# Optimization experiments

Hardware: AMD Instinct MI355X
Metric: run time of the kernel (lower is better)

The kernel has to match this reference:

```python
import jax, jax.numpy as jnp
import numpy as np
import math

EMBED_DIM = 256
NUM_HEADS = 8
HEAD_DIM = EMBED_DIM // NUM_HEADS
SEQ = 512
BSZ = 2


def setup_inputs() -> dict:
    key = jax.random.key(0)
    ks = jax.random.split(key, 9)
    def xavier(k, shape):
        fan_in, fan_out = shape[1], shape[0]
        bound = math.sqrt(6.0 / (fan_in + fan_out))
        return jax.random.uniform(k, shape, jnp.float32, -bound, bound)
    return {
        "query": jax.random.normal(ks[0], (SEQ, BSZ, EMBED_DIM), jnp.float32),
        "key": jax.random.normal(ks[1], (SEQ, BSZ, EMBED_DIM), jnp.float32),
        "value": jax.random.normal(ks[2], (SEQ, BSZ, EMBED_DIM), jnp.float32),
        "rel_pos_embedding": jax.random.normal(ks[3], (BSZ, SEQ, SEQ, EMBED_DIM), jnp.float32),
        "attn_mask": jax.random.normal(ks[4], (SEQ, SEQ), jnp.float32),
        "in_proj_weight": xavier(ks[5], (3 * EMBED_DIM, EMBED_DIM)),
        "in_proj_bias": jnp.zeros((3 * EMBED_DIM,), jnp.float32),
        "out_proj_weight": xavier(ks[6], (EMBED_DIM, EMBED_DIM)),
        "out_proj_bias": jnp.zeros((EMBED_DIM,), jnp.float32),
    }


def reference(query, key, value, rel_pos_embedding, attn_mask,
              in_proj_weight, in_proj_bias, out_proj_weight, out_proj_bias):
    L, B, E = query.shape
    H, D = NUM_HEADS, HEAD_DIM
    # NOTE: original module projects ONLY the query and chunks into q,k,v
    qkv = query @ in_proj_weight.T + in_proj_bias          # (L,B,3E)
    q, k, v = jnp.split(qkv, 3, axis=-1)                    # each (L,B,E)
    # (L,B,E) -> (B*H, L, D)
    def to_heads(t):
        return jnp.swapaxes(t.reshape(L, B * H, D), 0, 1)
    q, k, v = to_heads(q), to_heads(k), to_heads(v)
    scores = jnp.einsum('nld,nmd->nlm', q, k) / math.sqrt(D)  # (B*H,L,L)
    # relative position bias: einsum over UNSCALED q
    q4 = q.reshape(B, H, L, D)
    rel = rel_pos_embedding.reshape(B, L, L, H, D)
    rel_bias = jnp.einsum('bhld,blmhd->bhlm', q4, rel)        # (B,H,L,L)
    scores = scores.reshape(B, H, L, L) + rel_bias
    # additive 2D attn_mask broadcast over batch and heads
    scores = scores + attn_mask[None, None, :, :]
    scores = scores.reshape(B * H, L, L)
    attn = jax.nn.softmax(scores, axis=-1)                    # (B*H,L,L)
    out = jnp.einsum('nlm,nmd->nld', attn, v)                 # (B*H,L,D)
    out = jnp.swapaxes(out, 0, 1).reshape(L, B, E)            # (L,B,E)
    out = out @ out_proj_weight.T + out_proj_bias
    return out, attn
```

## Files before the change

### kernel.cpp

```cpp
#include <hip/hip_runtime.h>
#include <math.h>

#define L_SEQ 512
#define BSZ 2
#define NH 8
#define HD 32
#define E 256
#define SCALE 0.17677669529663687f
#define SROW 520

typedef float f32x4 __attribute__((ext_vector_type(4)));

template <int CTRL>
__device__ __forceinline__ float dpp_add(float x) {
    return x + __int_as_float(
        __builtin_amdgcn_update_dpp(0, __float_as_int(x), CTRL, 0xF, 0xF, true));
}
__device__ __forceinline__ float octet_allsum(float x) {
    x = dpp_add<0xB1>(x);
    x = dpp_add<0x4E>(x);
    x = dpp_add<0x141>(x);
    return x;
}


__global__ void inproj_kernel(const float* __restrict__ query,
                              const float* __restrict__ W,
                              const float* __restrict__ bias,
                              float* __restrict__ q2,
                              float* __restrict__ kh,
                              float* __restrict__ vh) {
    int r0 = blockIdx.x * 4;
    int y  = blockIdx.y;
    int t = threadIdx.x;
    __shared__ float xs[4][E];
#pragma unroll
    for (int r = 0; r < 4; ++r) xs[r][t] = query[(size_t)(r0 + r) * E + t];
    __syncthreads();

    int c = t & 7, cg = t >> 3;
#pragma unroll
    for (int pp = 0; pp < 4; ++pp) {
        int pass = y * 4 + pp;
        int col = pass * 32 + cg;
        float a[3][4];
#pragma unroll
        for (int p = 0; p < 3; ++p)
#pragma unroll
            for (int r = 0; r < 4; ++r) a[p][r] = 0.f;

#pragma unroll
        for (int kk = 0; kk < 8; ++kk) {
            float4 x0 = ((const float4*)xs[0])[c + kk * 8];
            float4 x1 = ((const float4*)xs[1])[c + kk * 8];
            float4 x2 = ((const float4*)xs[2])[c + kk * 8];
            float4 x3 = ((const float4*)xs[3])[c + kk * 8];
#pragma unroll
            for (int p = 0; p < 3; ++p) {
                float4 w = ((const float4*)(W + (size_t)(p * E + col) * E))[c + kk * 8];
                a[p][0] += w.x * x0.x + w.y * x0.y + w.z * x0.z + w.w * x0.w;
                a[p][1] += w.x * x1.x + w.y * x1.y + w.z * x1.z + w.w * x1.w;
                a[p][2] += w.x * x2.x + w.y * x2.y + w.z * x2.z + w.w * x2.w;
                a[p][3] += w.x * x3.x + w.y * x3.y + w.z * x3.z + w.w * x3.w;
            }
        }
#pragma unroll
        for (int p = 0; p < 3; ++p)
#pragma unroll
            for (int r = 0; r < 4; ++r) a[p][r] = octet_allsum(a[p][r]);

        if (c == 0) {
#pragma unroll
            for (int p = 0; p < 3; ++p) {
                float bb = bias[p * E + col];
#pragma unroll
                for (int r = 0; r < 4; ++r) {
                    int row = r0 + r, l = row >> 1, b = row & 1;
                    float val = a[p][r] + bb;
                    if (p == 0) {
                        q2[((size_t)b * L_SEQ + l) * E + col] = val;
                    } else {
                        int h = col >> 5, d = col & 31;
                        float* dst = (p == 1) ? kh : vh;
                        dst[((size_t)(b * NH + h) * L_SEQ + l) * HD + d] = val;
                    }
                }
            }
        }
    }
}

__global__ void qk_kernel(const float* __restrict__ q2,
                          const float* __restrict__ kh,
                          const float* __restrict__ mask,
                          float* __restrict__ scores) {
    int n = blockIdx.x;
    int b = n >> 3, h = n & 7;
    int l0 = blockIdx.y * 32;
    int t = threadIdx.x, lane = t & 63, w = t >> 6;

    __shared__ float qs[32][32];
    {
        int row = t >> 3, quad = t & 7;
        float4 qv = *(const float4*)(q2 + ((size_t)b * L_SEQ + l0 + row) * E + h * HD + quad * 4);
        ((float4*)qs[row])[quad] = qv;
    }
    __syncthreads();

    f32x4 ka[8], kb[8];
    const float* kbase = kh + (size_t)n * L_SEQ * HD;
    {
        const f32x4* pa = (const f32x4*)(kbase + (size_t)(w * 128 + lane) * HD);
        const f32x4* pb = (const f32x4*)(kbase + (size_t)(w * 128 + 64 + lane) * HD);
#pragma unroll
        for (int i = 0; i < 8; ++i) { ka[i] = pa[i]; kb[i] = pb[i]; }
    }

    for (int li = 0; li < 32; ++li) {
        int l = l0 + li;
        float da = 0.f, db = 0.f;
#pragma unroll
        for (int i = 0; i < 8; ++i) {
            float4 qv = ((const float4*)qs[li])[i];
            da += ka[i].x * qv.x + ka[i].y * qv.y + ka[i].z * qv.z + ka[i].w * qv.w;
            db += kb[i].x * qv.x + kb[i].y * qv.y + kb[i].z * qv.z + kb[i].w * qv.w;
        }
        size_t off = ((size_t)n * L_SEQ + l) * L_SEQ;
        const float* mrow = mask + (size_t)l * L_SEQ;
        scores[off + w * 128 + lane]      = da * SCALE + mrow[w * 128 + lane];
        scores[off + w * 128 + 64 + lane] = db * SCALE + mrow[w * 128 + 64 + lane];
    }
}

__global__ void attn_kernel(const float* __restrict__ q2,
                            const float* __restrict__ vh,
                            const float* __restrict__ rpe,
                            const float* __restrict__ scores,
                            float* __restrict__ attn_out,
                            float* __restrict__ oh2) {
    int bid = blockIdx.x;
    int b = bid >> 9, l = bid & (L_SEQ - 1);
    int t = threadIdx.x;
    int lane = t & 63, wid = t >> 6;

    __shared__ float qs[E];
    __shared__ float s_lds[NH * SROW];

    if (t < E) qs[t] = q2[((size_t)b * L_SEQ + l) * E + t];
    __syncthreads();

    f32x4 qc = ((const f32x4*)qs)[lane];
    int csel = lane & 7, h1 = lane >> 3;
    const float* rbase = rpe + ((size_t)(b * L_SEQ + l)) * L_SEQ * E;

    for (int ii = 0; ii < 8; ++ii) {
        float keep = 0.f;
#pragma unroll
        for (int i8 = 0; i8 < 8; ++i8) {
            int m = wid * 64 + ii * 8 + i8;
            f32x4 rv = __builtin_nontemporal_load(((const f32x4*)(rbase + (size_t)m * E)) + lane);
            float part = rv.x * qc.x + rv.y * qc.y + rv.z * qc.z + rv.w * qc.w;
            part = octet_allsum(part);
            keep = (i8 == csel) ? part : keep;
        }
        s_lds[h1 * SROW + wid * 64 + ii * 8 + csel] = keep;
    }
    __syncthreads();

    int h = wid;
    const float* srow = scores + ((size_t)(b * NH + h) * L_SEQ + l) * L_SEQ;
    float sv[8];
    float mx = -1e30f;
#pragma unroll
    for (int i = 0; i < 8; ++i) {
        int m = i * 64 + lane;
        sv[i] = s_lds[h * SROW + m] + srow[m];
        mx = fmaxf(mx, sv[i]);
    }
#pragma unroll
    for (int off = 32; off > 0; off >>= 1) mx = fmaxf(mx, __shfl_xor(mx, off));
    float sum = 0.f;
#pragma unroll
    for (int i = 0; i < 8; ++i) { sv[i] = __expf(sv[i] - mx); sum += sv[i]; }
#pragma unroll
    for (int off = 32; off > 0; off >>= 1) sum += __shfl_xor(sum, off);
    float inv = 1.0f / sum;

    float* arow = attn_out + ((size_t)(b * NH + h) * L_SEQ + l) * L_SEQ;
#pragma unroll
    for (int i = 0; i < 8; ++i) {
        int m = i * 64 + lane;
        float pn = sv[i] * inv;
        arow[m] = pn;
        s_lds[h * SROW + m] = pn;
    }

    int dq = lane & 7, mg = lane >> 3;
    const f32x4* vbase = (const f32x4*)(vh + (size_t)(b * NH + h) * L_SEQ * HD);
    float4 acc = {0.f, 0.f, 0.f, 0.f};
#pragma unroll 4
    for (int i = 0; i < 64; ++i) {
        int m = i * 8 + mg;
        f32x4 v4 = vbase[(size_t)m * 8 + dq];
        float p = s_lds[h * SROW + m];
        acc.x += p * v4.x; acc.y += p * v4.y; acc.z += p * v4.z; acc.w += p * v4.w;
    }
#pragma unroll
    for (int off = 8; off <= 32; off <<= 1) {
        acc.x += __shfl_xor(acc.x, off);
        acc.y += __shfl_xor(acc.y, off);
        acc.z += __shfl_xor(acc.z, off);
        acc.w += __shfl_xor(acc.w, off);
    }
    if (mg == 0) {
        ((float4*)(oh2 + ((size_t)b * L_SEQ + l) * E))[h * 8 + dq] = acc;
    }
}

__global__ void outproj_kernel(const float* __restrict__ oh2,
                               const float* __restrict__ W,
                               const float* __restrict__ bias,
                               float* __restrict__ out) {
    int r0 = blockIdx.x * 4;
    int y  = blockIdx.y;
    int t = threadIdx.x;
    __shared__ float xs[4][E];
#pragma unroll
    for (int r = 0; r < 4; ++r) {
        int row = r0 + r, l = row >> 1, b = row & 1;
        xs[r][t] = oh2[((size_t)b * L_SEQ + l) * E + t];
    }
    __syncthreads();

    int c = t & 7, cg = t >> 3;
#pragma unroll
    for (int pp = 0; pp < 4; ++pp) {
        int pass = y * 4 + pp;
        int col = pass * 32 + cg;
        const float4* wp = (const float4*)(W + (size_t)col * E);
        float a0 = 0.f, a1 = 0.f, a2 = 0.f, a3 = 0.f;
#pragma unroll
        for (int kk = 0; kk < 8; ++kk) {
            float4 w  = wp[c + kk * 8];
            float4 x0 = ((const float4*)xs[0])[c + kk * 8];
            float4 x1 = ((const float4*)xs[1])[c + kk * 8];
            float4 x2 = ((const float4*)xs[2])[c + kk * 8];
            float4 x3 = ((const float4*)xs[3])[c + kk * 8];
            a0 += w.x * x0.x + w.y * x0.y + w.z * x0.z + w.w * x0.w;
            a1 += w.x * x1.x + w.y * x1.y + w.z * x1.z + w.w * x1.w;
            a2 += w.x * x2.x + w.y * x2.y + w.z * x2.z + w.w * x2.w;
            a3 += w.x * x3.x + w.y * x3.y + w.z * x3.z + w.w * x3.w;
        }
        a0 = octet_allsum(a0); a1 = octet_allsum(a1);
        a2 = octet_allsum(a2); a3 = octet_allsum(a3);
        if (c == 0) {
            float bb = bias[col];
            float res[4] = {a0, a1, a2, a3};
#pragma unroll
            for (int r = 0; r < 4; ++r) {
                out[(size_t)(r0 + r) * E + col] = res[r] + bb;
            }
        }
    }
}

extern "C" void kernel_launch(void* const* d_in, const int* in_sizes, int n_in,
                              void* d_out, int out_size, void* d_ws, size_t ws_size,
                              hipStream_t stream) {
    const float* query = (const float*)d_in[0];
    const float* rpe   = (const float*)d_in[3];
    const float* mask  = (const float*)d_in[4];
    const float* Win   = (const float*)d_in[5];
    const float* bin   = (const float*)d_in[6];
    const float* Wout  = (const float*)d_in[7];
    const float* bout  = (const float*)d_in[8];

    float* out  = (float*)d_out;
    float* attn = (float*)d_out + (size_t)L_SEQ * BSZ * E;

    float* q2     = (float*)d_ws;
    float* kh     = q2  + (size_t)BSZ * L_SEQ * E;
    float* vh     = kh  + (size_t)BSZ * NH * L_SEQ * HD;
    float* oh2    = vh  + (size_t)BSZ * NH * L_SEQ * HD;
    float* scores = oh2 + (size_t)BSZ * L_SEQ * E;

    inproj_kernel<<<dim3((L_SEQ * BSZ) / 4, 2), E, 0, stream>>>(query, Win, bin, q2, kh, vh);
    qk_kernel<<<dim3(BSZ * NH, L_SEQ / 32), 256, 0, stream>>>(q2, kh, mask, scores);
    attn_kernel<<<BSZ * L_SEQ, 512, 0, stream>>>(q2, vh, rpe, scores, attn, oh2);
    outproj_kernel<<<dim3((L_SEQ * BSZ) / 4, 2), E, 0, stream>>>(oh2, Wout, bout, out);
}
```

Measured before the change: 188.5 us.

## Split PV out of attention kernel, widen projection grids, simplify rel-pos reduction

Moves the attention-times-V product out of the fused attention kernel into a separate pv_kernel. The new kernel stages V in LDS with a swizzle and re-reads the attn rows that were just written. The in/out projection and QK kernels get more blocks with less work each, and DPP octet sums are replaced by shfl_xor. The rel-pos loop now uses plain loads instead of nontemporal loads and writes from one lane per octet. The rpe stream is still the dominant cost, and the extra launch plus the attn re-read add traffic.

```diff
diff --git a/kernel.cpp b/kernel.cpp
--- a/kernel.cpp
+++ b/kernel.cpp
@@ -11,18 +11,6 @@
 
 typedef float f32x4 __attribute__((ext_vector_type(4)));
 
-template <int CTRL>
-__device__ __forceinline__ float dpp_add(float x) {
-    return x + __int_as_float(
-        __builtin_amdgcn_update_dpp(0, __float_as_int(x), CTRL, 0xF, 0xF, true));
-}
-__device__ __forceinline__ float octet_allsum(float x) {
-    x = dpp_add<0xB1>(x);
-    x = dpp_add<0x4E>(x);
-    x = dpp_add<0x141>(x);
-    return x;
-}
-
 
 __global__ void inproj_kernel(const float* __restrict__ query,
                               const float* __restrict__ W,
@@ -30,214 +18,19 @@
                               float* __restrict__ q2,
                               float* __restrict__ kh,
                               float* __restrict__ vh) {
-    int r0 = blockIdx.x * 4;
-    int y  = blockIdx.y;
+    int rg = blockIdx.x;
+    int cg3 = blockIdx.y;
     int t = threadIdx.x;
     __shared__ float xs[4][E];
 #pragma unroll
-    for (int r = 0; r < 4; ++r) xs[r][t] = query[(size_t)(r0 + r) * E + t];
+    for (int r = 0; r < 4; ++r) xs[r][t] = query[(size_t)(rg * 4 + r) * E + t];
     __syncthreads();
 
     int c = t & 7, cg = t >> 3;
 #pragma unroll
-    for (int pp = 0; pp < 4; ++pp) {
-        int pass = y * 4 + pp;
-        int col = pass * 32 + cg;
-        float a[3][4];
-#pragma unroll
-        for (int p = 0; p < 3; ++p)
-#pragma unroll
-            for (int r = 0; r < 4; ++r) a[p][r] = 0.f;
-
-#pragma unroll
-        for (int kk = 0; kk < 8; ++kk) {
-            float4 x0 = ((const float4*)xs[0])[c + kk * 8];
-            float4 x1 = ((const float4*)xs[1])[c + kk * 8];
-            float4 x2 = ((const float4*)xs[2])[c + kk * 8];
-            float4 x3 = ((const float4*)xs[3])[c + kk * 8];
-#pragma unroll
-            for (int p = 0; p < 3; ++p) {
-                float4 w = ((const float4*)(W + (size_t)(p * E + col) * E))[c + kk * 8];
-                a[p][0] += w.x * x0.x + w.y * x0.y + w.z * x0.z + w.w * x0.w;
-                a[p][1] += w.x * x1.x + w.y * x1.y + w.z * x1.z + w.w * x1.w;
-                a[p][2] += w.x * x2.x + w.y * x2.y + w.z * x2.z + w.w * x2.w;
-                a[p][3] += w.x * x3.x + w.y * x3.y + w.z * x3.z + w.w * x3.w;
-            }
-        }
-#pragma unroll
-        for (int p = 0; p < 3; ++p)
-#pragma unroll
-            for (int r = 0; r < 4; ++r) a[p][r] = octet_allsum(a[p][r]);
-
-        if (c == 0) {
-#pragma unroll
-            for (int p = 0; p < 3; ++p) {
-                float bb = bias[p * E + col];
-#pragma unroll
-                for (int r = 0; r < 4; ++r) {
-                    int row = r0 + r, l = row >> 1, b = row & 1;
-                    float val = a[p][r] + bb;
-                    if (p == 0) {
-                        q2[((size_t)b * L_SEQ + l) * E + col] = val;
-                    } else {
-                        int h = col >> 5, d = col & 31;
-                        float* dst = (p == 1) ? kh : vh;
-                        dst[((size_t)(b * NH + h) * L_SEQ + l) * HD + d] = val;
-                    }
-                }
-            }
-        }
-    }
-}
-
-__global__ void qk_kernel(const float* __restrict__ q2,
-                          const float* __restrict__ kh,
-                          const float* __restrict__ mask,
-                          float* __restrict__ scores) {
-    int n = blockIdx.x;
-    int b = n >> 3, h = n & 7;
-    int l0 = blockIdx.y * 32;
-    int t = threadIdx.x, lane = t & 63, w = t >> 6;
-
-    __shared__ float qs[32][32];
-    {
-        int row = t >> 3, quad = t & 7;
-        float4 qv = *(const float4*)(q2 + ((size_t)b * L_SEQ + l0 + row) * E + h * HD + quad * 4);
-        ((float4*)qs[row])[quad] = qv;
-    }
-    __syncthreads();
-
-    f32x4 ka[8], kb[8];
-    const float* kbase = kh + (size_t)n * L_SEQ * HD;
-    {
-        const f32x4* pa = (const f32x4*)(kbase + (size_t)(w * 128 + lane) * HD);
-        const f32x4* pb = (const f32x4*)(kbase + (size_t)(w * 128 + 64 + lane) * HD);
-#pragma unroll
-        for (int i = 0; i < 8; ++i) { ka[i] = pa[i]; kb[i] = pb[i]; }
-    }
-
-    for (int li = 0; li < 32; ++li) {
-        int l = l0 + li;
-        float da = 0.f, db = 0.f;
-#pragma unroll
-        for (int i = 0; i < 8; ++i) {
-            float4 qv = ((const float4*)qs[li])[i];
-            da += ka[i].x * qv.x + ka[i].y * qv.y + ka[i].z * qv.z + ka[i].w * qv.w;
-            db += kb[i].x * qv.x + kb[i].y * qv.y + kb[i].z * qv.z + kb[i].w * qv.w;
-        }
-        size_t off = ((size_t)n * L_SEQ + l) * L_SEQ;
-        const float* mrow = mask + (size_t)l * L_SEQ;
-        scores[off + w * 128 + lane]      = da * SCALE + mrow[w * 128 + lane];
-        scores[off + w * 128 + 64 + lane] = db * SCALE + mrow[w * 128 + 64 + lane];
-    }
-}
-
-__global__ void attn_kernel(const float* __restrict__ q2,
-                            const float* __restrict__ vh,
-                            const float* __restrict__ rpe,
-                            const float* __restrict__ scores,
-                            float* __restrict__ attn_out,
-                            float* __restrict__ oh2) {
-    int bid = blockIdx.x;
-    int b = bid >> 9, l = bid & (L_SEQ - 1);
-    int t = threadIdx.x;
-    int lane = t & 63, wid = t >> 6;
-
-    __shared__ float qs[E];
-    __shared__ float s_lds[NH * SROW];
-
-    if (t < E) qs[t] = q2[((size_t)b * L_SEQ + l) * E + t];
-    __syncthreads();
-
-    f32x4 qc = ((const f32x4*)qs)[lane];
-    int csel = lane & 7, h1 = lane >> 3;
-    const float* rbase = rpe + ((size_t)(b * L_SEQ + l)) * L_SEQ * E;
-
-    for (int ii = 0; ii < 8; ++ii) {
-        float keep = 0.f;
-#pragma unroll
-        for (int i8 = 0; i8 < 8; ++i8) {
-            int m = wid * 64 + ii * 8 + i8;
-            f32x4 rv = __builtin_nontemporal_load(((const f32x4*)(rbase + (size_t)m * E)) + lane);
-            float part = rv.x * qc.x + rv.y * qc.y + rv.z * qc.z + rv.w * qc.w;
-            part = octet_allsum(part);
-            keep = (i8 == csel) ? part : keep;
-        }
-        s_lds[h1 * SROW + wid * 64 + ii * 8 + csel] = keep;
-    }
-    __syncthreads();
-
-    int h = wid;
-    const float* srow = scores + ((size_t)(b * NH + h) * L_SEQ + l) * L_SEQ;
-    float sv[8];
-    float mx = -1e30f;
-#pragma unroll
-    for (int i = 0; i < 8; ++i) {
-        int m = i * 64 + lane;
-        sv[i] = s_lds[h * SROW + m] + srow[m];
-        mx = fmaxf(mx, sv[i]);
-    }
-#pragma unroll
-    for (int off = 32; off > 0; off >>= 1) mx = fmaxf(mx, __shfl_xor(mx, off));
-    float sum = 0.f;
-#pragma unroll
-    for (int i = 0; i < 8; ++i) { sv[i] = __expf(sv[i] - mx); sum += sv[i]; }
-#pragma unroll
-    for (int off = 32; off > 0; off >>= 1) sum += __shfl_xor(sum, off);
-    float inv = 1.0f / sum;
-
-    float* arow = attn_out + ((size_t)(b * NH + h) * L_SEQ + l) * L_SEQ;
-#pragma unroll
-    for (int i = 0; i < 8; ++i) {
-        int m = i * 64 + lane;
-        float pn = sv[i] * inv;
-        arow[m] = pn;
-        s_lds[h * SROW + m] = pn;
-    }
-
-    int dq = lane & 7, mg = lane >> 3;
-    const f32x4* vbase = (const f32x4*)(vh + (size_t)(b * NH + h) * L_SEQ * HD);
-    float4 acc = {0.f, 0.f, 0.f, 0.f};
-#pragma unroll 4
-    for (int i = 0; i < 64; ++i) {
-        int m = i * 8 + mg;
-        f32x4 v4 = vbase[(size_t)m * 8 + dq];
-        float p = s_lds[h * SROW + m];
-        acc.x += p * v4.x; acc.y += p * v4.y; acc.z += p * v4.z; acc.w += p * v4.w;
-    }
-#pragma unroll
-    for (int off = 8; off <= 32; off <<= 1) {
-        acc.x += __shfl_xor(acc.x, off);
-        acc.y += __shfl_xor(acc.y, off);
-        acc.z += __shfl_xor(acc.z, off);
-        acc.w += __shfl_xor(acc.w, off);
-    }
-    if (mg == 0) {
-        ((float4*)(oh2 + ((size_t)b * L_SEQ + l) * E))[h * 8 + dq] = acc;
-    }
-}
-
-__global__ void outproj_kernel(const float* __restrict__ oh2,
-                               const float* __restrict__ W,
-                               const float* __restrict__ bias,
-                               float* __restrict__ out) {
-    int r0 = blockIdx.x * 4;
-    int y  = blockIdx.y;
-    int t = threadIdx.x;
-    __shared__ float xs[4][E];
-#pragma unroll
-    for (int r = 0; r < 4; ++r) {
-        int row = r0 + r, l = row >> 1, b = row & 1;
-        xs[r][t] = oh2[((size_t)b * L_SEQ + l) * E + t];
-    }
-    __syncthreads();
-
-    int c = t & 7, cg = t >> 3;
-#pragma unroll
-    for (int pp = 0; pp < 4; ++pp) {
-        int pass = y * 4 + pp;
-        int col = pass * 32 + cg;
-        const float4* wp = (const float4*)(W + (size_t)col * E);
+    for (int pp = 0; pp < 2; ++pp) {
+        int col768 = cg3 * 64 + pp * 32 + cg;
+        const float4* wp = (const float4*)(W + (size_t)col768 * E);
         float a0 = 0.f, a1 = 0.f, a2 = 0.f, a3 = 0.f;
 #pragma unroll
         for (int kk = 0; kk < 8; ++kk) {
@@ -251,14 +44,234 @@
             a2 += w.x * x2.x + w.y * x2.y + w.z * x2.z + w.w * x2.w;
             a3 += w.x * x3.x + w.y * x3.y + w.z * x3.z + w.w * x3.w;
         }
-        a0 = octet_allsum(a0); a1 = octet_allsum(a1);
-        a2 = octet_allsum(a2); a3 = octet_allsum(a3);
+#pragma unroll
+        for (int off = 1; off <= 4; off <<= 1) {
+            a0 += __shfl_xor(a0, off);
+            a1 += __shfl_xor(a1, off);
+            a2 += __shfl_xor(a2, off);
+            a3 += __shfl_xor(a3, off);
+        }
+        if (c == 0) {
+            int p = col768 >> 8, col = col768 & 255;
+            float bb = bias[col768];
+            float res[4] = {a0, a1, a2, a3};
+#pragma unroll
+            for (int r = 0; r < 4; ++r) {
+                int row = rg * 4 + r, l = row >> 1, b = row & 1;
+                float val = res[r] + bb;
+                if (p == 0) {
+                    q2[((size_t)b * L_SEQ + l) * E + col] = val;
+                } else {
+                    int h = col >> 5, d = col & 31;
+                    float* dst = (p == 1) ? kh : vh;
+                    dst[((size_t)(b * NH + h) * L_SEQ + l) * HD + d] = val;
+                }
+            }
+        }
+    }
+}
+
+__global__ void qk_kernel(const float* __restrict__ q2,
+                          const float* __restrict__ kh,
+                          const float* __restrict__ mask,
+                          float* __restrict__ scores) {
+    int n = blockIdx.x;
+    int b = n >> 3, h = n & 7;
+    int l0 = blockIdx.y * 8;
+    int t = threadIdx.x, lane = t & 63, w = t >> 6;
+
+    __shared__ float qs[8][32];
+    if (t < 64) {
+        int row = t >> 3, quad = t & 7;
+        float4 qv = *(const float4*)(q2 + ((size_t)b * L_SEQ + l0 + row) * E + h * HD + quad * 4);
+        ((float4*)qs[row])[quad] = qv;
+    }
+    __syncthreads();
+
+    f32x4 ka[8], kb[8];
+    const float* kbase = kh + (size_t)n * L_SEQ * HD;
+    {
+        const f32x4* pa = (const f32x4*)(kbase + (size_t)(w * 128 + lane) * HD);
+        const f32x4* pb = (const f32x4*)(kbase + (size_t)(w * 128 + 64 + lane) * HD);
+#pragma unroll
+        for (int i = 0; i < 8; ++i) { ka[i] = pa[i]; kb[i] = pb[i]; }
+    }
+
+#pragma unroll
+    for (int li = 0; li < 8; ++li) {
+        int l = l0 + li;
+        float da = 0.f, db = 0.f;
+#pragma unroll
+        for (int i = 0; i < 8; ++i) {
+            float4 qv = ((const float4*)qs[li])[i];
+            da += ka[i].x * qv.x + ka[i].y * qv.y + ka[i].z * qv.z + ka[i].w * qv.w;
+            db += kb[i].x * qv.x + kb[i].y * qv.y + kb[i].z * qv.z + kb[i].w * qv.w;
+        }
+        size_t off = ((size_t)n * L_SEQ + l) * L_SEQ;
+        const float* mrow = mask + (size_t)l * L_SEQ;
+        scores[off + w * 128 + lane]      = da * SCALE + mrow[w * 128 + lane];
+        scores[off + w * 128 + 64 + lane] = db * SCALE + mrow[w * 128 + 64 + lane];
+    }
+}
+
+__global__ void relattn_kernel(const float* __restrict__ q2,
+                               const float* __restrict__ rpe,
+                               const float* __restrict__ scores,
+                               float* __restrict__ attn_out) {
+    int bid = blockIdx.x;
+    int b = bid >> 9, l = bid & (L_SEQ - 1);
+    int t = threadIdx.x;
+    int lane = t & 63, wid = t >> 6;
+
+    __shared__ float qs[E];
+    __shared__ float s_lds[NH * SROW];
+
+    if (t < E) qs[t] = q2[((size_t)b * L_SEQ + l) * E + t];
+    __syncthreads();
+
+    f32x4 qc = ((const f32x4*)qs)[lane];
+    int h1 = lane >> 3;
+    const float* rbase = rpe + ((size_t)(b * L_SEQ + l)) * L_SEQ * E;
+
+#pragma unroll 8
+    for (int i = 0; i < 64; ++i) {
+        int m = wid * 64 + i;
+        f32x4 rv = *(((const f32x4*)(rbase + (size_t)m * E)) + lane);
+        float part = rv.x * qc.x + rv.y * qc.y + rv.z * qc.z + rv.w * qc.w;
+        part += __shfl_xor(part, 1);
+        part += __shfl_xor(part, 2);
+        part += __shfl_xor(part, 4);
+        if ((lane & 7) == 0) s_lds[h1 * SROW + m] = part;
+    }
+    __syncthreads();
+
+    int h = wid;
+    const float* srow = scores + ((size_t)(b * NH + h) * L_SEQ + l) * L_SEQ;
+    float sv[8];
+    float mx = -1e30f;
+#pragma unroll
+    for (int i = 0; i < 8; ++i) {
+        int m = i * 64 + lane;
+        sv[i] = s_lds[h * SROW + m] + srow[m];
+        mx = fmaxf(mx, sv[i]);
+    }
+#pragma unroll
+    for (int off = 32; off > 0; off >>= 1) mx = fmaxf(mx, __shfl_xor(mx, off));
+    float sum = 0.f;
+#pragma unroll
+    for (int i = 0; i < 8; ++i) { sv[i] = __expf(sv[i] - mx); sum += sv[i]; }
+#pragma unroll
+    for (int off = 32; off > 0; off >>= 1) sum += __shfl_xor(sum, off);
+    float inv = 1.0f / sum;
+
+    float* arow = attn_out + ((size_t)(b * NH + h) * L_SEQ + l) * L_SEQ;
+#pragma unroll
+    for (int i = 0; i < 8; ++i) {
+        arow[i * 64 + lane] = sv[i] * inv;
+    }
+}
+
+__global__ void pv_kernel(const float* __restrict__ attn,
+                          const float* __restrict__ vh,
+                          float* __restrict__ oh2) {
+    int n = blockIdx.x;
+    int b = n >> 3, h = n & 7;
+    int lg = blockIdx.y;
+    int t = threadIdx.x;
+
+    __shared__ float vlds[L_SEQ * HD];
+    __shared__ float pl[L_SEQ];
+    __shared__ float red[32][33];
+
+    const f32x4* vsrc = (const f32x4*)(vh + (size_t)n * L_SEQ * HD);
+#pragma unroll
+    for (int j = 0; j < 16; ++j) {
+        int qg = j * 256 + t;
+        int m = qg >> 3, dq = qg & 7;
+        f32x4 v4 = vsrc[qg];
+        int qsw = dq ^ (m & 7);
+        *(f32x4*)&vlds[m * HD + qsw * 4] = v4;
+    }
+    __syncthreads();
+
+    int mg = t >> 3, dq = t & 7;
+    int qsw = dq ^ (mg & 7);
+    for (int li = 0; li < 16; ++li) {
+        int l = lg * 16 + li;
+        const float2* prow = (const float2*)(attn + ((size_t)n * L_SEQ + l) * L_SEQ);
+        *(float2*)&pl[t * 2] = prow[t];
+        __syncthreads();
+
+        float ax = 0.f, ay = 0.f, az = 0.f, aw = 0.f;
+#pragma unroll
+        for (int i = 0; i < 16; ++i) {
+            int m = i * 32 + mg;
+            f32x4 v4 = *(const f32x4*)&vlds[m * HD + qsw * 4];
+            float p = pl[m];
+            ax += p * v4.x; ay += p * v4.y; az += p * v4.z; aw += p * v4.w;
+        }
+        red[mg][dq * 4 + 0] = ax;
+        red[mg][dq * 4 + 1] = ay;
+        red[mg][dq * 4 + 2] = az;
+        red[mg][dq * 4 + 3] = aw;
+        __syncthreads();
+
+        if (t < 32) {
+            float s = 0.f;
+#pragma unroll
+            for (int g = 0; g < 32; ++g) s += red[g][t];
+            oh2[((size_t)b * L_SEQ + l) * E + h * HD + t] = s;
+        }
+        __syncthreads();
+    }
+}
+
+__global__ void outproj_kernel(const float* __restrict__ oh2,
+                               const float* __restrict__ W,
+                               const float* __restrict__ bias,
+                               float* __restrict__ out) {
+    int rg = blockIdx.x;
+    int cg3 = blockIdx.y;
+    int t = threadIdx.x;
+    __shared__ float xs[4][E];
+#pragma unroll
+    for (int r = 0; r < 4; ++r) {
+        int row = rg * 4 + r, l = row >> 1, b = row & 1;
+        xs[r][t] = oh2[((size_t)b * L_SEQ + l) * E + t];
+    }
+    __syncthreads();
+
+    int c = t & 7, cg = t >> 3;
+#pragma unroll
+    for (int pp = 0; pp < 2; ++pp) {
+        int col = cg3 * 64 + pp * 32 + cg;
+        const float4* wp = (const float4*)(W + (size_t)col * E);
+        float a0 = 0.f, a1 = 0.f, a2 = 0.f, a3 = 0.f;
+#pragma unroll
+        for (int kk = 0; kk < 8; ++kk) {
+            float4 w  = wp[c + kk * 8];
+            float4 x0 = ((const float4*)xs[0])[c + kk * 8];
+            float4 x1 = ((const float4*)xs[1])[c + kk * 8];
+            float4 x2 = ((const float4*)xs[2])[c + kk * 8];
+            float4 x3 = ((const float4*)xs[3])[c + kk * 8];
+            a0 += w.x * x0.x + w.y * x0.y + w.z * x0.z + w.w * x0.w;
+            a1 += w.x * x1.x + w.y * x1.y + w.z * x1.z + w.w * x1.w;
+            a2 += w.x * x2.x + w.y * x2.y + w.z * x2.z + w.w * x2.w;
+            a3 += w.x * x3.x + w.y * x3.y + w.z * x3.z + w.w * x3.w;
+        }
+#pragma unroll
+        for (int off = 1; off <= 4; off <<= 1) {
+            a0 += __shfl_xor(a0, off);
+            a1 += __shfl_xor(a1, off);
+            a2 += __shfl_xor(a2, off);
+            a3 += __shfl_xor(a3, off);
+        }
         if (c == 0) {
             float bb = bias[col];
             float res[4] = {a0, a1, a2, a3};
 #pragma unroll
             for (int r = 0; r < 4; ++r) {
-                out[(size_t)(r0 + r) * E + col] = res[r] + bb;
+                out[(size_t)(rg * 4 + r) * E + col] = res[r] + bb;
             }
         }
     }
@@ -284,8 +297,9 @@
     float* oh2    = vh  + (size_t)BSZ * NH * L_SEQ * HD;
     float* scores = oh2 + (size_t)BSZ * L_SEQ * E;
 
-    inproj_kernel<<<dim3((L_SEQ * BSZ) / 4, 2), E, 0, stream>>>(query, Win, bin, q2, kh, vh);
-    qk_kernel<<<dim3(BSZ * NH, L_SEQ / 32), 256, 0, stream>>>(q2, kh, mask, scores);
-    attn_kernel<<<BSZ * L_SEQ, 512, 0, stream>>>(q2, vh, rpe, scores, attn, oh2);
-    outproj_kernel<<<dim3((L_SEQ * BSZ) / 4, 2), E, 0, stream>>>(oh2, Wout, bout, out);
-}
+    inproj_kernel<<<dim3(256, 12), 256, 0, stream>>>(query, Win, bin, q2, kh, vh);
+    qk_kernel<<<dim3(BSZ * NH, 64), 256, 0, stream>>>(q2, kh, mask, scores);
+    relattn_kernel<<<BSZ * L_SEQ, 512, 0, stream>>>(q2, rpe, scores, attn);
+    pv_kernel<<<dim3(BSZ * NH, 32), 256, 0, stream>>>(attn, vh, oh2);
+    outproj_kernel<<<dim3(256, 4), 256, 0, stream>>>(oh2, Wout, bout, out);
+}
```

Result: faster. 167.6 us (-11.1%).
